# Optimization experiments

Hardware: AMD Instinct MI355X
Metric: run time of the kernel (lower is better)

Reference implementation:

```python
import jax, jax.numpy as jnp
import numpy as np

HIDDEN = 1024
FFN = 4096
N_EXPERTS = 8
TOP_K = 2


def setup_inputs() -> dict:
    key = jax.random.key(0)
    ks = jax.random.split(key, 6)
    x = jax.random.normal(ks[0], (2, 2048, HIDDEN), dtype=jnp.float32)
    Wr = jax.random.normal(ks[1], (N_EXPERTS, HIDDEN), dtype=jnp.float32) * 0.02
    W1 = jax.random.normal(ks[2], (N_EXPERTS, FFN, HIDDEN), dtype=jnp.float32) * 0.02
    b1 = jnp.zeros((N_EXPERTS, FFN), dtype=jnp.float32)
    W2 = jax.random.normal(ks[3], (N_EXPERTS, HIDDEN, FFN), dtype=jnp.float32) * 0.02
    b2 = jnp.zeros((N_EXPERTS, HIDDEN), dtype=jnp.float32)
    return {"x": x, "Wr": Wr, "W1": W1, "b1": b1, "W2": W2, "b2": b2}


def reference(x, Wr, W1, b1, W2, b2):
    # x: [B, S, D]; Wr: [E, D]; W1: [E, F, D]; W2: [E, D, F]
    B, S, D = x.shape
    E = Wr.shape[0]
    xf = x.reshape(-1, D)                              # [T, D]
    T = xf.shape[0]
    logits = xf @ Wr.T                                 # [T, E]
    probs = jax.nn.softmax(logits, axis=-1)
    top_v, top_i = jax.lax.top_k(probs, TOP_K)         # [T, K]
    top_v = top_v / jnp.sum(top_v, axis=-1, keepdims=True)
    # combine weights: zero except the top-k experts per token
    comb = jnp.zeros((T, E), dtype=xf.dtype).at[jnp.arange(T)[:, None], top_i].add(top_v)
    # run every expert densely (same math as gather/FFN/weighted-scatter)
    h = jax.nn.gelu(jnp.einsum('td,efd->etf', xf, W1) + b1[:, None, :], approximate=False)  # [E, T, F]
    y = jnp.einsum('etf,edf->etd', h, W2) + b2[:, None, :]                                   # [E, T, D]
    out = jnp.einsum('etd,te->td', y, comb)            # weighted combine
    return out.reshape(B, S, D)
```

## Files before the change

### kernel.cpp

```cpp
#include <hip/hip_runtime.h>

#define HIDDEN 1024
#define FFN    4096
#define NEXP   8
#define TOKENS 4096
#define ASSIGN 8192

typedef __attribute__((ext_vector_type(8))) short s8v;
typedef __attribute__((ext_vector_type(4))) float f4v;

__device__ __forceinline__ float bf2f(ushort u) {
    return __uint_as_float(((unsigned int)u) << 16);
}
__device__ __forceinline__ ushort f2bf(float f) {
    unsigned int x = __float_as_uint(f);
    return (ushort)((x + 0x7fffu + ((x >> 16) & 1u)) >> 16);
}

#define GLDS16(g, l) __builtin_amdgcn_global_load_lds( \
    (const __attribute__((address_space(1))) unsigned int*)(g), \
    (__attribute__((address_space(3))) unsigned int*)(l), 16, 0, 0)

__device__ __forceinline__ int swz_scol(int t) {
    const int srow = t >> 2, c = t & 3;
    return ((c ^ ((srow >> 1) & 3)) << 3);
}
__device__ __forceinline__ int lds_off(int row, int lq) {
    return row * 32 + ((lq ^ ((row >> 1) & 3)) << 3);
}

#define KBODY(it, bA, bB, sA, sB)                                               \
  {                                                                             \
    if ((it) == NT - 1) { asm volatile("s_waitcnt vmcnt(0)" ::: "memory"); }    \
    else                { asm volatile("s_waitcnt vmcnt(4)" ::: "memory"); }    \
    __builtin_amdgcn_s_barrier();                                               \
    __builtin_amdgcn_sched_barrier(0);                                          \
    if ((it) + 2 < NT) {                                                        \
      const int kn_ = ((it) + 2) * 32;                                          \
      GLDS16(gA0 + kn_, (sA) + wv * 512);                                       \
      GLDS16(gA1 + kn_, (sA) + 2048 + wv * 512);                                \
      GLDS16(gB0 + kn_, (sB) + wv * 512);                                       \
      GLDS16(gB1 + kn_, (sB) + 2048 + wv * 512);                                \
    }                                                                           \
    s8v a_[4], b_[4];                                                           \
    _Pragma("unroll")                                                           \
    for (int i_ = 0; i_ < 4; ++i_)                                              \
      a_[i_] = *(const s8v*)((bA) + lds_off(row_off + i_ * 16 + l15, lq));      \
    _Pragma("unroll")                                                           \
    for (int j_ = 0; j_ < 4; ++j_)                                              \
      b_[j_] = *(const s8v*)((bB) + lds_off(col_off + j_ * 16 + l15, lq));      \
    _Pragma("unroll")                                                           \
    for (int i_ = 0; i_ < 4; ++i_)                                              \
      _Pragma("unroll")                                                         \
      for (int j_ = 0; j_ < 4; ++j_)                                            \
        acc[i_][j_] = __builtin_amdgcn_mfma_f32_16x16x32_bf16(a_[i_], b_[j_],   \
                                                              acc[i_][j_], 0, 0, 0); \
  }

__global__ void conv_kernel(const float4* __restrict__ src, ushort4* __restrict__ dst) {
    const int i = blockIdx.x * blockDim.x + threadIdx.x;
    const float4 v = src[i];
    ushort4 o;
    o.x = f2bf(v.x); o.y = f2bf(v.y); o.z = f2bf(v.z); o.w = f2bf(v.w);
    dst[i] = o;
}

__global__ void router_kernel(const float* __restrict__ x, const float* __restrict__ Wr,
                              int* __restrict__ counts, int* __restrict__ topk_idx,
                              float* __restrict__ topk_w) {
    const int tok  = blockIdx.x;
    const int lane = threadIdx.x;
    float acc[NEXP];
#pragma unroll
    for (int e = 0; e < NEXP; ++e) acc[e] = 0.f;
#pragma unroll
    for (int i = 0; i < HIDDEN / 64; ++i) {
        const int idx = i * 64 + lane;
        const float xv = x[(size_t)tok * HIDDEN + idx];
#pragma unroll
        for (int e = 0; e < NEXP; ++e) acc[e] += xv * Wr[e * HIDDEN + idx];
    }
#pragma unroll
    for (int e = 0; e < NEXP; ++e) {
#pragma unroll
        for (int off = 32; off > 0; off >>= 1) acc[e] += __shfl_xor(acc[e], off);
    }
    if (lane == 0) {
        int i0 = 0;
        for (int e = 1; e < NEXP; ++e) if (acc[e] > acc[i0]) i0 = e;
        int i1 = (i0 == 0) ? 1 : 0;
        for (int e = 0; e < NEXP; ++e) if (e != i0 && acc[e] > acc[i1]) i1 = e;
        const float e1 = expf(acc[i1] - acc[i0]);
        const float s  = 1.f + e1;
        topk_idx[tok * 2 + 0] = i0;
        topk_idx[tok * 2 + 1] = i1;
        topk_w[tok * 2 + 0]   = 1.f / s;
        topk_w[tok * 2 + 1]   = e1 / s;
        atomicAdd(&counts[i0], 1);
        atomicAdd(&counts[i1], 1);
    }
}

__global__ void prefix_kernel(const int* __restrict__ counts, int* __restrict__ offsets,
                              int* __restrict__ cursors) {
    if (threadIdx.x == 0) {
        int s = 0;
        for (int e = 0; e < NEXP; ++e) { offsets[e] = s; cursors[e] = s; s += counts[e]; }
        offsets[NEXP] = s;
    }
}

__global__ void scatter_kernel(const int* __restrict__ topk_idx, const float* __restrict__ topk_w,
                               int* __restrict__ cursors, int* __restrict__ token_list,
                               float* __restrict__ weight_list, int* __restrict__ slot_of) {
    const int a = blockIdx.x * blockDim.x + threadIdx.x;
    if (a >= ASSIGN) return;
    const int e   = topk_idx[a];
    const int pos = atomicAdd(&cursors[e], 1);
    token_list[pos]  = a >> 1;
    weight_list[pos] = topk_w[a];
    slot_of[a]       = pos;
}

__global__ __launch_bounds__(256)
void gemm1_kernel(const ushort* __restrict__ x, const ushort* __restrict__ W1,
                  const float* __restrict__ b1, const int* __restrict__ token_list,
                  const int* __restrict__ counts, const int* __restrict__ offsets,
                  ushort* __restrict__ h) {
    const int bid    = blockIdx.x;
    const int e      = bid & 7;
    const int r      = bid >> 3;
    const int tile_m = r & 63;
    const int tile_n = r >> 6;
    const int n_e    = counts[e];
    if (n_e <= 0 || tile_m * 128 >= n_e) return;
    const int base   = offsets[e];

    __shared__ __align__(16) ushort As[3 * 128 * 32];
    __shared__ __align__(16) ushort Bs[3 * 128 * 32];

    const int t    = threadIdx.x;
    const int lane = t & 63;
    const int wv   = t >> 6;
    const int srow = t >> 2;
    const int scol = swz_scol(t);

    const int r0 = tile_m * 128 + srow;
    const int r1 = r0 + 64;
    const int tokA0 = token_list[base + (r0 < n_e ? r0 : n_e - 1)];
    const int tokA1 = token_list[base + (r1 < n_e ? r1 : n_e - 1)];
    const ushort* gA0 = x + (size_t)tokA0 * HIDDEN + scol;
    const ushort* gA1 = x + (size_t)tokA1 * HIDDEN + scol;
    const ushort* gB0 = W1 + ((size_t)e * FFN + tile_n * 128 + srow) * HIDDEN + scol;
    const ushort* gB1 = W1 + ((size_t)e * FFN + tile_n * 128 + 64 + srow) * HIDDEN + scol;

    f4v acc[4][4];
#pragma unroll
    for (int i = 0; i < 4; ++i)
#pragma unroll
        for (int j = 0; j < 4; ++j) { f4v z = {0.f, 0.f, 0.f, 0.f}; acc[i][j] = z; }

    const int row_off = (wv & 1) * 64;
    const int col_off = (wv >> 1) * 64;
    const int l15 = lane & 15;
    const int lq  = lane >> 4;

    const int NT = HIDDEN / 32;

    GLDS16(gA0,      As + wv * 512);
    GLDS16(gA1,      As + 2048 + wv * 512);
    GLDS16(gB0,      Bs + wv * 512);
    GLDS16(gB1,      Bs + 2048 + wv * 512);
    GLDS16(gA0 + 32, As + 4096 + wv * 512);
    GLDS16(gA1 + 32, As + 4096 + 2048 + wv * 512);
    GLDS16(gB0 + 32, Bs + 4096 + wv * 512);
    GLDS16(gB1 + 32, Bs + 4096 + 2048 + wv * 512);

    for (int it0 = 0; it0 < NT; it0 += 3) {
        KBODY(it0,     As,        Bs,        As + 8192, Bs + 8192);
        if (it0 + 1 < NT) KBODY(it0 + 1, As + 4096, Bs + 4096, As,        Bs);
        if (it0 + 2 < NT) KBODY(it0 + 2, As + 8192, Bs + 8192, As + 4096, Bs + 4096);
    }

    const int mrem = n_e - tile_m * 128;
#pragma unroll
    for (int i = 0; i < 4; ++i) {
#pragma unroll
        for (int rr = 0; rr < 4; ++rr) {
            const int m_loc = row_off + i * 16 + lq * 4 + rr;
            if (m_loc < mrem) {
                const size_t hrow = (size_t)(base + tile_m * 128 + m_loc) * FFN;
#pragma unroll
                for (int j = 0; j < 4; ++j) {
                    const int colF = tile_n * 128 + col_off + j * 16 + l15;
                    float v = acc[i][j][rr] + b1[e * FFN + colF];
                    v = 0.5f * v * (1.0f + erff(v * 0.70710678118654752f));
                    h[hrow + colF] = f2bf(v);
                }
            }
        }
    }
}

__global__ __launch_bounds__(256)
void gemm2_kernel(const ushort* __restrict__ h, const ushort* __restrict__ W2,
                  const float* __restrict__ b2, const float* __restrict__ weight_list,
                  const int* __restrict__ counts, const int* __restrict__ offsets,
                  ushort* __restrict__ y) {
    const int bid    = blockIdx.x;
    const int e      = bid & 7;
    const int r      = bid >> 3;
    const int tile_m = r & 63;
    const int tile_n = r >> 6;
    const int n_e    = counts[e];
    if (n_e <= 0 || tile_m * 128 >= n_e) return;
    const int base   = offsets[e];

    __shared__ __align__(16) ushort As[3 * 128 * 32];
    __shared__ __align__(16) ushort Bs[3 * 128 * 32];

    const int t    = threadIdx.x;
    const int lane = t & 63;
    const int wv   = t >> 6;
    const int srow = t >> 2;
    const int scol = swz_scol(t);

    const int r0 = tile_m * 128 + srow;
    const int r1 = r0 + 64;
    const int slot0 = base + (r0 < n_e ? r0 : n_e - 1);
    const int slot1 = base + (r1 < n_e ? r1 : n_e - 1);
    const ushort* gA0 = h + (size_t)slot0 * FFN + scol;
    const ushort* gA1 = h + (size_t)slot1 * FFN + scol;
    const ushort* gB0 = W2 + ((size_t)e * HIDDEN + tile_n * 128 + srow) * FFN + scol;
    const ushort* gB1 = W2 + ((size_t)e * HIDDEN + tile_n * 128 + 64 + srow) * FFN + scol;

    f4v acc[4][4];
#pragma unroll
    for (int i = 0; i < 4; ++i)
#pragma unroll
        for (int j = 0; j < 4; ++j) { f4v z = {0.f, 0.f, 0.f, 0.f}; acc[i][j] = z; }

    const int row_off = (wv & 1) * 64;
    const int col_off = (wv >> 1) * 64;
    const int l15 = lane & 15;
    const int lq  = lane >> 4;

    const int NT = FFN / 32;

    GLDS16(gA0,      As + wv * 512);
    GLDS16(gA1,      As + 2048 + wv * 512);
    GLDS16(gB0,      Bs + wv * 512);
    GLDS16(gB1,      Bs + 2048 + wv * 512);
    GLDS16(gA0 + 32, As + 4096 + wv * 512);
    GLDS16(gA1 + 32, As + 4096 + 2048 + wv * 512);
    GLDS16(gB0 + 32, Bs + 4096 + wv * 512);
    GLDS16(gB1 + 32, Bs + 4096 + 2048 + wv * 512);

    for (int it0 = 0; it0 < NT; it0 += 3) {
        KBODY(it0,     As,        Bs,        As + 8192, Bs + 8192);
        if (it0 + 1 < NT) KBODY(it0 + 1, As + 4096, Bs + 4096, As,        Bs);
        if (it0 + 2 < NT) KBODY(it0 + 2, As + 8192, Bs + 8192, As + 4096, Bs + 4096);
    }

    const int mrem = n_e - tile_m * 128;
#pragma unroll
    for (int i = 0; i < 4; ++i) {
#pragma unroll
        for (int rr = 0; rr < 4; ++rr) {
            const int m_loc = row_off + i * 16 + lq * 4 + rr;
            if (m_loc < mrem) {
                const int slot = base + tile_m * 128 + m_loc;
                const float wgt = weight_list[slot];
#pragma unroll
                for (int j = 0; j < 4; ++j) {
                    const int colD = tile_n * 128 + col_off + j * 16 + l15;
                    const float v = acc[i][j][rr] + b2[e * HIDDEN + colD];
                    y[(size_t)slot * HIDDEN + colD] = f2bf(v * wgt);
                }
            }
        }
    }
}

__global__ void combine_kernel(const int* __restrict__ slot_of, const ushort* __restrict__ y,
                               float* __restrict__ out) {
    const int idx = blockIdx.x * blockDim.x + threadIdx.x;
    const int t = idx >> 8;
    const int d = (idx & 255) * 4;
    const int s0 = slot_of[t * 2 + 0];
    const int s1 = slot_of[t * 2 + 1];
    const ushort4 a = *(const ushort4*)(y + (size_t)s0 * HIDDEN + d);
    const ushort4 b = *(const ushort4*)(y + (size_t)s1 * HIDDEN + d);
    float4 o;
    o.x = bf2f(a.x) + bf2f(b.x);
    o.y = bf2f(a.y) + bf2f(b.y);
    o.z = bf2f(a.z) + bf2f(b.z);
    o.w = bf2f(a.w) + bf2f(b.w);
    *(float4*)(out + (size_t)t * HIDDEN + d) = o;
}

extern "C" void kernel_launch(void* const* d_in, const int* in_sizes, int n_in,
                              void* d_out, int out_size, void* d_ws, size_t ws_size,
                              hipStream_t stream) {
    const float* x  = (const float*)d_in[0];
    const float* Wr = (const float*)d_in[1];
    const float* W1 = (const float*)d_in[2];
    const float* b1 = (const float*)d_in[3];
    const float* W2 = (const float*)d_in[4];
    const float* b2 = (const float*)d_in[5];
    float* out = (float*)d_out;

    char* ws = (char*)d_ws;
    int*    counts      = (int*)(ws + 0);
    int*    offsets     = (int*)(ws + 256);
    int*    cursors     = (int*)(ws + 512);
    int*    topk_idx    = (int*)(ws + 1024);
    float*  topk_w      = (float*)(ws + 1024 + 32768);
    int*    slot_of     = (int*)(ws + 1024 + 65536);
    int*    token_list  = (int*)(ws + 1024 + 98304);
    float*  weight_list = (float*)(ws + 1024 + 131072);
    ushort* x_bf        = (ushort*)(ws + (1 << 20));
    ushort* wbuf        = (ushort*)(ws + (1 << 20) + 8388608);
    ushort* h           = (ushort*)(ws + (1 << 20) + 8388608 + 67108864);
    ushort* y           = (ushort*)(ws + (1 << 20) + 8388608 + 2 * 67108864ull);

    const int NW = NEXP * FFN * HIDDEN;

    hipMemsetAsync(counts, 0, 64, stream);
    conv_kernel<<<(TOKENS * HIDDEN / 4) / 256, 256, 0, stream>>>((const float4*)x, (ushort4*)x_bf);
    conv_kernel<<<(NW / 4) / 256, 256, 0, stream>>>((const float4*)W1, (ushort4*)wbuf);

    router_kernel<<<TOKENS, 64, 0, stream>>>(x, Wr, counts, topk_idx, topk_w);
    prefix_kernel<<<1, 64, 0, stream>>>(counts, offsets, cursors);
    scatter_kernel<<<ASSIGN / 256, 256, 0, stream>>>(topk_idx, topk_w, cursors,
                                                     token_list, weight_list, slot_of);

    gemm1_kernel<<<NEXP * 64 * (FFN / 128), 256, 0, stream>>>(
        x_bf, wbuf, b1, token_list, counts, offsets, h);

    conv_kernel<<<(NW / 4) / 256, 256, 0, stream>>>((const float4*)W2, (ushort4*)wbuf);

    gemm2_kernel<<<NEXP * 64 * (HIDDEN / 128), 256, 0, stream>>>(
        h, wbuf, b2, weight_list, counts, offsets, y);

    combine_kernel<<<(TOKENS * HIDDEN / 4) / 256, 256, 0, stream>>>(slot_of, y, out);
}
```

Measured before the change: 696.3 us.

## Compact tile list, deepen LDS pipeline, fuse combine via atomics, fast GeLU

The prefix kernel now builds a compact list of (expert, m-tile) entries, so the GEMM grids launch only useful tiles instead of many early-exit blocks. Both GEMMs move from a 3-stage to a 4-stage LDS ring with prefetch distance 3, and raise wave priority around the MFMA block. GEMM2 now atomically adds the weighted result into a zeroed fp32 output, which removes the y buffer and the combine kernel. GeLU uses a polynomial erf approximation instead of erff. The atomics make summation order nondeterministic, and the extra LDS may lower occupancy.

```diff
diff --git a/kernel.cpp b/kernel.cpp
--- a/kernel.cpp
+++ b/kernel.cpp
@@ -5,6 +5,7 @@
 #define NEXP   8
 #define TOKENS 4096
 #define ASSIGN 8192
+#define NENT   72
 
 typedef __attribute__((ext_vector_type(8))) short s8v;
 typedef __attribute__((ext_vector_type(4))) float f4v;
@@ -17,6 +18,18 @@
     return (ushort)((x + 0x7fffu + ((x >> 16) & 1u)) >> 16);
 }
 
+__device__ __forceinline__ float gelu_f(float v) {
+    const float u = v * 0.70710678118654752f;
+    const float a = fabsf(u);
+    const float t = 1.0f / fmaf(0.3275911f, a, 1.0f);
+    const float p = t * (0.254829592f + t * (-0.284496736f + t * (1.421413741f +
+                     t * (-1.453152027f + t * 1.061405429f))));
+    const float ex = __expf(-u * u);
+    float er = 1.0f - p * ex;
+    er = (u < 0.f) ? -er : er;
+    return 0.5f * v * (1.0f + er);
+}
+
 #define GLDS16(g, l) __builtin_amdgcn_global_load_lds( \
     (const __attribute__((address_space(1))) unsigned int*)(g), \
     (__attribute__((address_space(3))) unsigned int*)(l), 16, 0, 0)
@@ -31,12 +44,13 @@
 
 #define KBODY(it, bA, bB, sA, sB)                                               \
   {                                                                             \
-    if ((it) == NT - 1) { asm volatile("s_waitcnt vmcnt(0)" ::: "memory"); }    \
-    else                { asm volatile("s_waitcnt vmcnt(4)" ::: "memory"); }    \
+    if ((it) == NT - 1)      { asm volatile("s_waitcnt vmcnt(0)" ::: "memory");}\
+    else if ((it) == NT - 2) { asm volatile("s_waitcnt vmcnt(4)" ::: "memory");}\
+    else                     { asm volatile("s_waitcnt vmcnt(8)" ::: "memory");}\
     __builtin_amdgcn_s_barrier();                                               \
     __builtin_amdgcn_sched_barrier(0);                                          \
-    if ((it) + 2 < NT) {                                                        \
-      const int kn_ = ((it) + 2) * 32;                                          \
+    if ((it) + 3 < NT) {                                                        \
+      const int kn_ = ((it) + 3) * 32;                                          \
       GLDS16(gA0 + kn_, (sA) + wv * 512);                                       \
       GLDS16(gA1 + kn_, (sA) + 2048 + wv * 512);                                \
       GLDS16(gB0 + kn_, (sB) + wv * 512);                                       \
@@ -49,12 +63,14 @@
     _Pragma("unroll")                                                           \
     for (int j_ = 0; j_ < 4; ++j_)                                              \
       b_[j_] = *(const s8v*)((bB) + lds_off(col_off + j_ * 16 + l15, lq));      \
+    __builtin_amdgcn_s_setprio(1);                                              \
     _Pragma("unroll")                                                           \
     for (int i_ = 0; i_ < 4; ++i_)                                              \
       _Pragma("unroll")                                                         \
       for (int j_ = 0; j_ < 4; ++j_)                                            \
         acc[i_][j_] = __builtin_amdgcn_mfma_f32_16x16x32_bf16(a_[i_], b_[j_],   \
                                                               acc[i_][j_], 0, 0, 0); \
+    __builtin_amdgcn_s_setprio(0);                                              \
   }
 
 __global__ void conv_kernel(const float4* __restrict__ src, ushort4* __restrict__ dst) {
@@ -102,42 +118,46 @@
 }
 
 __global__ void prefix_kernel(const int* __restrict__ counts, int* __restrict__ offsets,
-                              int* __restrict__ cursors) {
+                              int* __restrict__ cursors, int* __restrict__ tiles) {
     if (threadIdx.x == 0) {
-        int s = 0;
-        for (int e = 0; e < NEXP; ++e) { offsets[e] = s; cursors[e] = s; s += counts[e]; }
+        int s = 0, nt = 0;
+        for (int e = 0; e < NEXP; ++e) {
+            offsets[e] = s; cursors[e] = s;
+            const int ne = counts[e];
+            for (int tm = 0; tm * 128 < ne; ++tm) tiles[nt++] = e | (tm << 8);
+            s += ne;
+        }
         offsets[NEXP] = s;
+        for (; nt < NENT; ++nt) tiles[nt] = -1;
     }
 }
 
 __global__ void scatter_kernel(const int* __restrict__ topk_idx, const float* __restrict__ topk_w,
                                int* __restrict__ cursors, int* __restrict__ token_list,
-                               float* __restrict__ weight_list, int* __restrict__ slot_of) {
+                               float* __restrict__ weight_list) {
     const int a = blockIdx.x * blockDim.x + threadIdx.x;
     if (a >= ASSIGN) return;
     const int e   = topk_idx[a];
     const int pos = atomicAdd(&cursors[e], 1);
     token_list[pos]  = a >> 1;
     weight_list[pos] = topk_w[a];
-    slot_of[a]       = pos;
 }
 
 __global__ __launch_bounds__(256)
 void gemm1_kernel(const ushort* __restrict__ x, const ushort* __restrict__ W1,
                   const float* __restrict__ b1, const int* __restrict__ token_list,
                   const int* __restrict__ counts, const int* __restrict__ offsets,
-                  ushort* __restrict__ h) {
-    const int bid    = blockIdx.x;
-    const int e      = bid & 7;
-    const int r      = bid >> 3;
-    const int tile_m = r & 63;
-    const int tile_n = r >> 6;
+                  const int* __restrict__ tiles, ushort* __restrict__ h) {
+    const int info = tiles[blockIdx.x];
+    if (info < 0) return;
+    const int e      = info & 255;
+    const int tile_m = info >> 8;
+    const int tile_n = blockIdx.y;
     const int n_e    = counts[e];
-    if (n_e <= 0 || tile_m * 128 >= n_e) return;
     const int base   = offsets[e];
 
-    __shared__ __align__(16) ushort As[3 * 128 * 32];
-    __shared__ __align__(16) ushort Bs[3 * 128 * 32];
+    __shared__ __align__(16) ushort As[4 * 128 * 32];
+    __shared__ __align__(16) ushort Bs[4 * 128 * 32];
 
     const int t    = threadIdx.x;
     const int lane = t & 63;
@@ -167,19 +187,19 @@
 
     const int NT = HIDDEN / 32;
 
-    GLDS16(gA0,      As + wv * 512);
-    GLDS16(gA1,      As + 2048 + wv * 512);
-    GLDS16(gB0,      Bs + wv * 512);
-    GLDS16(gB1,      Bs + 2048 + wv * 512);
-    GLDS16(gA0 + 32, As + 4096 + wv * 512);
-    GLDS16(gA1 + 32, As + 4096 + 2048 + wv * 512);
-    GLDS16(gB0 + 32, Bs + 4096 + wv * 512);
-    GLDS16(gB1 + 32, Bs + 4096 + 2048 + wv * 512);
-
-    for (int it0 = 0; it0 < NT; it0 += 3) {
-        KBODY(it0,     As,        Bs,        As + 8192, Bs + 8192);
-        if (it0 + 1 < NT) KBODY(it0 + 1, As + 4096, Bs + 4096, As,        Bs);
-        if (it0 + 2 < NT) KBODY(it0 + 2, As + 8192, Bs + 8192, As + 4096, Bs + 4096);
+#pragma unroll
+    for (int p = 0; p < 3; ++p) {
+        GLDS16(gA0 + p * 32, As + p * 4096 + wv * 512);
+        GLDS16(gA1 + p * 32, As + p * 4096 + 2048 + wv * 512);
+        GLDS16(gB0 + p * 32, Bs + p * 4096 + wv * 512);
+        GLDS16(gB1 + p * 32, Bs + p * 4096 + 2048 + wv * 512);
+    }
+
+    for (int it0 = 0; it0 < NT; it0 += 4) {
+        KBODY(it0 + 0, As + 0 * 4096, Bs + 0 * 4096, As + 3 * 4096, Bs + 3 * 4096);
+        KBODY(it0 + 1, As + 1 * 4096, Bs + 1 * 4096, As + 0 * 4096, Bs + 0 * 4096);
+        KBODY(it0 + 2, As + 2 * 4096, Bs + 2 * 4096, As + 1 * 4096, Bs + 1 * 4096);
+        KBODY(it0 + 3, As + 3 * 4096, Bs + 3 * 4096, As + 2 * 4096, Bs + 2 * 4096);
     }
 
     const int mrem = n_e - tile_m * 128;
@@ -193,8 +213,7 @@
 #pragma unroll
                 for (int j = 0; j < 4; ++j) {
                     const int colF = tile_n * 128 + col_off + j * 16 + l15;
-                    float v = acc[i][j][rr] + b1[e * FFN + colF];
-                    v = 0.5f * v * (1.0f + erff(v * 0.70710678118654752f));
+                    const float v = gelu_f(acc[i][j][rr] + b1[e * FFN + colF]);
                     h[hrow + colF] = f2bf(v);
                 }
             }
@@ -205,19 +224,19 @@
 __global__ __launch_bounds__(256)
 void gemm2_kernel(const ushort* __restrict__ h, const ushort* __restrict__ W2,
                   const float* __restrict__ b2, const float* __restrict__ weight_list,
-                  const int* __restrict__ counts, const int* __restrict__ offsets,
-                  ushort* __restrict__ y) {
-    const int bid    = blockIdx.x;
-    const int e      = bid & 7;
-    const int r      = bid >> 3;
-    const int tile_m = r & 63;
-    const int tile_n = r >> 6;
+                  const int* __restrict__ token_list, const int* __restrict__ counts,
+                  const int* __restrict__ offsets, const int* __restrict__ tiles,
+                  float* __restrict__ out) {
+    const int info = tiles[blockIdx.x];
+    if (info < 0) return;
+    const int e      = info & 255;
+    const int tile_m = info >> 8;
+    const int tile_n = blockIdx.y;
     const int n_e    = counts[e];
-    if (n_e <= 0 || tile_m * 128 >= n_e) return;
     const int base   = offsets[e];
 
-    __shared__ __align__(16) ushort As[3 * 128 * 32];
-    __shared__ __align__(16) ushort Bs[3 * 128 * 32];
+    __shared__ __align__(16) ushort As[4 * 128 * 32];
+    __shared__ __align__(16) ushort Bs[4 * 128 * 32];
 
     const int t    = threadIdx.x;
     const int lane = t & 63;
@@ -247,19 +266,19 @@
 
     const int NT = FFN / 32;
 
-    GLDS16(gA0,      As + wv * 512);
-    GLDS16(gA1,      As + 2048 + wv * 512);
-    GLDS16(gB0,      Bs + wv * 512);
-    GLDS16(gB1,      Bs + 2048 + wv * 512);
-    GLDS16(gA0 + 32, As + 4096 + wv * 512);
-    GLDS16(gA1 + 32, As + 4096 + 2048 + wv * 512);
-    GLDS16(gB0 + 32, Bs + 4096 + wv * 512);
-    GLDS16(gB1 + 32, Bs + 4096 + 2048 + wv * 512);
-
-    for (int it0 = 0; it0 < NT; it0 += 3) {
-        KBODY(it0,     As,        Bs,        As + 8192, Bs + 8192);
-        if (it0 + 1 < NT) KBODY(it0 + 1, As + 4096, Bs + 4096, As,        Bs);
-        if (it0 + 2 < NT) KBODY(it0 + 2, As + 8192, Bs + 8192, As + 4096, Bs + 4096);
+#pragma unroll
+    for (int p = 0; p < 3; ++p) {
+        GLDS16(gA0 + p * 32, As + p * 4096 + wv * 512);
+        GLDS16(gA1 + p * 32, As + p * 4096 + 2048 + wv * 512);
+        GLDS16(gB0 + p * 32, Bs + p * 4096 + wv * 512);
+        GLDS16(gB1 + p * 32, Bs + p * 4096 + 2048 + wv * 512);
+    }
+
+    for (int it0 = 0; it0 < NT; it0 += 4) {
+        KBODY(it0 + 0, As + 0 * 4096, Bs + 0 * 4096, As + 3 * 4096, Bs + 3 * 4096);
+        KBODY(it0 + 1, As + 1 * 4096, Bs + 1 * 4096, As + 0 * 4096, Bs + 0 * 4096);
+        KBODY(it0 + 2, As + 2 * 4096, Bs + 2 * 4096, As + 1 * 4096, Bs + 1 * 4096);
+        KBODY(it0 + 3, As + 3 * 4096, Bs + 3 * 4096, As + 2 * 4096, Bs + 2 * 4096);
     }
 
     const int mrem = n_e - tile_m * 128;
@@ -269,34 +288,18 @@
         for (int rr = 0; rr < 4; ++rr) {
             const int m_loc = row_off + i * 16 + lq * 4 + rr;
             if (m_loc < mrem) {
-                const int slot = base + tile_m * 128 + m_loc;
+                const int slot  = base + tile_m * 128 + m_loc;
                 const float wgt = weight_list[slot];
+                const int   tok = token_list[slot];
 #pragma unroll
                 for (int j = 0; j < 4; ++j) {
                     const int colD = tile_n * 128 + col_off + j * 16 + l15;
                     const float v = acc[i][j][rr] + b2[e * HIDDEN + colD];
-                    y[(size_t)slot * HIDDEN + colD] = f2bf(v * wgt);
+                    atomicAdd(&out[(size_t)tok * HIDDEN + colD], v * wgt);
                 }
             }
         }
     }
-}
-
-__global__ void combine_kernel(const int* __restrict__ slot_of, const ushort* __restrict__ y,
-                               float* __restrict__ out) {
-    const int idx = blockIdx.x * blockDim.x + threadIdx.x;
-    const int t = idx >> 8;
-    const int d = (idx & 255) * 4;
-    const int s0 = slot_of[t * 2 + 0];
-    const int s1 = slot_of[t * 2 + 1];
-    const ushort4 a = *(const ushort4*)(y + (size_t)s0 * HIDDEN + d);
-    const ushort4 b = *(const ushort4*)(y + (size_t)s1 * HIDDEN + d);
-    float4 o;
-    o.x = bf2f(a.x) + bf2f(b.x);
-    o.y = bf2f(a.y) + bf2f(b.y);
-    o.z = bf2f(a.z) + bf2f(b.z);
-    o.w = bf2f(a.w) + bf2f(b.w);
-    *(float4*)(out + (size_t)t * HIDDEN + d) = o;
 }
 
 extern "C" void kernel_launch(void* const* d_in, const int* in_sizes, int n_in,
@@ -314,34 +317,32 @@
     int*    counts      = (int*)(ws + 0);
     int*    offsets     = (int*)(ws + 256);
     int*    cursors     = (int*)(ws + 512);
-    int*    topk_idx    = (int*)(ws + 1024);
-    float*  topk_w      = (float*)(ws + 1024 + 32768);
-    int*    slot_of     = (int*)(ws + 1024 + 65536);
-    int*    token_list  = (int*)(ws + 1024 + 98304);
-    float*  weight_list = (float*)(ws + 1024 + 131072);
+    int*    tiles       = (int*)(ws + 768);
+    int*    topk_idx    = (int*)(ws + 2048);
+    float*  topk_w      = (float*)(ws + 2048 + 32768);
+    int*    token_list  = (int*)(ws + 2048 + 65536);
+    float*  weight_list = (float*)(ws + 2048 + 98304);
     ushort* x_bf        = (ushort*)(ws + (1 << 20));
     ushort* wbuf        = (ushort*)(ws + (1 << 20) + 8388608);
     ushort* h           = (ushort*)(ws + (1 << 20) + 8388608 + 67108864);
-    ushort* y           = (ushort*)(ws + (1 << 20) + 8388608 + 2 * 67108864ull);
 
     const int NW = NEXP * FFN * HIDDEN;
 
     hipMemsetAsync(counts, 0, 64, stream);
+    hipMemsetAsync(out, 0, (size_t)TOKENS * HIDDEN * 4, stream);
     conv_kernel<<<(TOKENS * HIDDEN / 4) / 256, 256, 0, stream>>>((const float4*)x, (ushort4*)x_bf);
     conv_kernel<<<(NW / 4) / 256, 256, 0, stream>>>((const float4*)W1, (ushort4*)wbuf);
 
     router_kernel<<<TOKENS, 64, 0, stream>>>(x, Wr, counts, topk_idx, topk_w);
-    prefix_kernel<<<1, 64, 0, stream>>>(counts, offsets, cursors);
+    prefix_kernel<<<1, 64, 0, stream>>>(counts, offsets, cursors, tiles);
     scatter_kernel<<<ASSIGN / 256, 256, 0, stream>>>(topk_idx, topk_w, cursors,
-                                                     token_list, weight_list, slot_of);
-
-    gemm1_kernel<<<NEXP * 64 * (FFN / 128), 256, 0, stream>>>(
-        x_bf, wbuf, b1, token_list, counts, offsets, h);
+                                                     token_list, weight_list);
+
+    gemm1_kernel<<<dim3(NENT, FFN / 128), 256, 0, stream>>>(
+        x_bf, wbuf, b1, token_list, counts, offsets, tiles, h);
 
     conv_kernel<<<(NW / 4) / 256, 256, 0, stream>>>((const float4*)W2, (ushort4*)wbuf);
 
-    gemm2_kernel<<<NEXP * 64 * (HIDDEN / 128), 256, 0, stream>>>(
-        h, wbuf, b2, weight_list, counts, offsets, y);
-
-    combine_kernel<<<(TOKENS * HIDDEN / 4) / 256, 256, 0, stream>>>(slot_of, y, out);
-}
+    gemm2_kernel<<<dim3(NENT, HIDDEN / 128), 256, 0, stream>>>(
+        h, wbuf, b2, weight_list, token_list, counts, offsets, tiles, out);
+}
```

After: 811.6 us. 16.6% more time.
